# Kernel tuning notes

Measured on AMD Instinct MI355X. Metric: run time of the kernel, lower is better.

## Reference

```python
import jax, jax.numpy as jnp
import numpy as np


def setup_inputs() -> dict:
    key = jax.random.key(0)
    k1, k2, k3, k4, k5 = jax.random.split(key, 5)
    B, S, ENC, DEC = 32, 2048, 1024, 512
    hidden = jax.random.normal(k1, (B, DEC), dtype=jnp.float32)
    encoder_outputs = jax.random.normal(k2, (B, S, ENC), dtype=jnp.float32)
    W = jax.random.normal(k3, (DEC, ENC + DEC), dtype=jnp.float32) * (1.0 / np.sqrt(ENC + DEC))
    b = jax.random.normal(k4, (DEC,), dtype=jnp.float32) * 0.01
    v = jax.random.uniform(k5, (DEC,), dtype=jnp.float32)  # torch.rand init
    return {"hidden": hidden, "encoder_outputs": encoder_outputs, "W": W, "b": b, "v": v}


def reference(hidden, encoder_outputs, W, b, v):
    # hidden: [B, D_dec], encoder_outputs: [B, S, D_enc]
    # Concat order in original: (hidden, encoder_outputs) -> split W accordingly.
    D_dec = hidden.shape[-1]
    Wh = W[:, :D_dec]   # [D_dec, D_dec] acts on hidden
    We = W[:, D_dec:]   # [D_dec, D_enc] acts on encoder_outputs
    # energy: tanh(Linear(cat(hidden_repeated, enc))) == tanh(h@Wh^T + enc@We^T + b)
    h_proj = jnp.einsum('bd,ed->be', hidden, Wh)                 # [B, D_dec]
    e_proj = jnp.einsum('bse,de->bsd', encoder_outputs, We)      # [B, S, D_dec]
    energy = jnp.tanh(e_proj + h_proj[:, None, :] + b)           # [B, S, D_dec]
    # scores: v . energy per (b, s); softmax over src_len
    scores = jnp.einsum('d,bsd->bs', v, energy)                  # [B, S]
    attn = jax.nn.softmax(scores, axis=-1)
    return attn[:, None, :]                                       # [B, 1, S]
```

## Files before the change

### kernel.cpp

```cpp
#include <hip/hip_runtime.h>
#include <hip/hip_bf16.h>


typedef __attribute__((ext_vector_type(8))) short bf16x8;
typedef __attribute__((ext_vector_type(4))) float f32x4;

__device__ __forceinline__ ushort f2bf(float x) {
    __hip_bfloat16 h = __float2bfloat16(x);
    return *reinterpret_cast<ushort*>(&h);
}

__device__ __forceinline__ bf16x8 pack8(float4 a, float4 b) {
    bf16x8 o;
    o[0] = (short)f2bf(a.x); o[1] = (short)f2bf(a.y);
    o[2] = (short)f2bf(a.z); o[3] = (short)f2bf(a.w);
    o[4] = (short)f2bf(b.x); o[5] = (short)f2bf(b.y);
    o[6] = (short)f2bf(b.z); o[7] = (short)f2bf(b.w);
    return o;
}

#define WS_WBF   0
#define WS_HB    (1u << 20)
#define WS_SCORE ((1u << 20) + (64u << 10))

__global__ void prep_kernel(const float* __restrict__ W,
                            const float* __restrict__ hidden,
                            const float* __restrict__ bias,
                            ushort* __restrict__ Wbf,
                            float* __restrict__ hb,
                            float* __restrict__ score) {
    const int bid = blockIdx.x, tid = threadIdx.x;
    if (bid < 512) {
        int idx = bid * 256 + tid;
        int d  = idx >> 8;
        int e4 = (idx & 255) * 4;
        float4 f = *(const float4*)(W + (size_t)d * 1536 + 512 + e4);
        ushort4 u;
        u.x = f2bf(f.x); u.y = f2bf(f.y); u.z = f2bf(f.z); u.w = f2bf(f.w);
        *(ushort4*)(Wbf + (size_t)d * 1024 + e4) = u;
    } else if (bid < 576) {
        int idx = (bid - 512) * 256 + tid;
        int b = idx >> 9, d = idx & 511;
        const float4* hp = (const float4*)(hidden + b * 512);
        const float4* wp = (const float4*)(W + (size_t)d * 1536);
        float acc = 0.f;
#pragma unroll 8
        for (int j = 0; j < 128; ++j) {
            float4 h = hp[j], w = wp[j];
            acc += h.x * w.x + h.y * w.y + h.z * w.z + h.w * w.w;
        }
        hb[idx] = acc + bias[d];
    } else {
        int idx = (bid - 576) * 256 + tid;
        float4 z = {0.f, 0.f, 0.f, 0.f};
        *(float4*)(score + (size_t)idx * 4) = z;
    }
}

__launch_bounds__(256, 3)
__global__ void eproj_scores(const float* __restrict__ enc,
                             const ushort* __restrict__ Wbf,
                             const float* __restrict__ hb,
                             const float* __restrict__ v,
                             float* __restrict__ scores) {
    __shared__ alignas(16) float Abuf[2][128 * 32];
    __shared__ float spart[2][128];

    const int tid  = threadIdx.x;
    const int lane = tid & 63, w = tid >> 6;
    const int wm = w >> 1, wn = w & 1;
    const int q = lane >> 4, ln = lane & 15;
    const int  nblk = blockIdx.x & 3;
    const long m0   = (long)(blockIdx.x >> 2) * 128;
    const int  bidx = (int)(m0 >> 11);
    const int  n0   = nblk * 128 + wn * 64;

    f32x4 acc[4][4];
#pragma unroll
    for (int mt = 0; mt < 4; ++mt)
#pragma unroll
        for (int nt = 0; nt < 4; ++nt)
            acc[mt][nt] = (f32x4){0.f, 0.f, 0.f, 0.f};

    const ushort* bptr[4];
#pragma unroll
    for (int nt = 0; nt < 4; ++nt)
        bptr[nt] = Wbf + (size_t)(n0 + nt * 16 + ln) * 1024 + q * 8;

    int sA0[4], sA1[4];
#pragma unroll
    for (int mt = 0; mt < 4; ++mt) {
        int rA = wm * 64 + mt * 16 + ln;
        sA0[mt] = (rA * 8 + ((2 * q)     ^ (rA & 7))) * 4;
        sA1[mt] = (rA * 8 + ((2 * q + 1) ^ (rA & 7))) * 4;
    }

#pragma unroll
    for (int i = 0; i < 4; ++i) {
        int s = i * 256 + tid;
        int r = s >> 3;
        int c = (s & 7) ^ (r & 7);
        const float* g = enc + (m0 + r) * 1024 + c * 4;
        float* lb = &Abuf[0][(i * 256 + w * 64) * 4];
        __builtin_amdgcn_global_load_lds(
            (const __attribute__((address_space(1))) void*)g,
            (__attribute__((address_space(3))) void*)lb, 16, 0, 0);
    }
    bf16x8 bfr[2][4];
#pragma unroll
    for (int nt = 0; nt < 4; ++nt)
        bfr[0][nt] = *(const bf16x8*)(bptr[nt]);

    int buf = 0;
#pragma unroll 2
    for (int kt = 0; kt < 32; ++kt) {
        const int p = kt & 1;
        __syncthreads();

        if (kt < 31) {
#pragma unroll
            for (int i = 0; i < 4; ++i) {
                int s = i * 256 + tid;
                int r = s >> 3;
                int c = (s & 7) ^ (r & 7);
                const float* g = enc + (m0 + r) * 1024 + (kt + 1) * 32 + c * 4;
                float* lb = &Abuf[buf ^ 1][(i * 256 + w * 64) * 4];
                __builtin_amdgcn_global_load_lds(
                    (const __attribute__((address_space(1))) void*)g,
                    (__attribute__((address_space(3))) void*)lb, 16, 0, 0);
            }
#pragma unroll
            for (int nt = 0; nt < 4; ++nt)
                bfr[p ^ 1][nt] = *(const bf16x8*)(bptr[nt] + (size_t)(kt + 1) * 32);
        }

        const float* Ab = Abuf[buf];
#pragma unroll
        for (int mt = 0; mt < 4; ++mt) {
            float4 a0 = *(const float4*)(Ab + sA0[mt]);
            float4 a1 = *(const float4*)(Ab + sA1[mt]);
            bf16x8 af = pack8(a0, a1);
#pragma unroll
            for (int nt = 0; nt < 4; ++nt)
                acc[mt][nt] = __builtin_amdgcn_mfma_f32_16x16x32_bf16(
                    af, bfr[p][nt], acc[mt][nt], 0, 0, 0);
        }
        buf ^= 1;
    }

    float partial[4][4];
#pragma unroll
    for (int mt = 0; mt < 4; ++mt)
#pragma unroll
        for (int r = 0; r < 4; ++r) partial[mt][r] = 0.f;

#pragma unroll
    for (int nt = 0; nt < 4; ++nt) {
        int d = n0 + nt * 16 + ln;
        float hbv = hb[bidx * 512 + d];
        float vv  = v[d];
#pragma unroll
        for (int mt = 0; mt < 4; ++mt)
#pragma unroll
            for (int r = 0; r < 4; ++r) {
                float x = acc[mt][nt][r] + hbv;
                float e = __expf(2.f * x);
                partial[mt][r] += vv * (1.f - 2.f / (e + 1.f));
            }
    }
#pragma unroll
    for (int mt = 0; mt < 4; ++mt)
#pragma unroll
        for (int r = 0; r < 4; ++r) {
            float s = partial[mt][r];
            s += __shfl_xor(s, 1);
            s += __shfl_xor(s, 2);
            s += __shfl_xor(s, 4);
            s += __shfl_xor(s, 8);
            partial[mt][r] = s;
        }
    if (ln == 0) {
#pragma unroll
        for (int mt = 0; mt < 4; ++mt)
#pragma unroll
            for (int r = 0; r < 4; ++r)
                spart[wn][wm * 64 + mt * 16 + q * 4 + r] = partial[mt][r];
    }
    __syncthreads();
    if (tid < 128)
        atomicAdd(&scores[m0 + tid], spart[0][tid] + spart[1][tid]);
}

__global__ void softmax_kernel(const float* __restrict__ scores, float* __restrict__ out) {
    int b = blockIdx.x;
    const float* sc = scores + b * 2048;
    __shared__ float wred[4], wsum[4];

    float lmax = -1e30f;
    for (int i = threadIdx.x; i < 2048; i += 256) lmax = fmaxf(lmax, sc[i]);
#pragma unroll
    for (int m = 1; m < 64; m <<= 1) lmax = fmaxf(lmax, __shfl_xor(lmax, m));
    if ((threadIdx.x & 63) == 0) wred[threadIdx.x >> 6] = lmax;
    __syncthreads();
    float gmax = fmaxf(fmaxf(wred[0], wred[1]), fmaxf(wred[2], wred[3]));

    float lsum = 0.f;
    for (int i = threadIdx.x; i < 2048; i += 256) lsum += __expf(sc[i] - gmax);
#pragma unroll
    for (int m = 1; m < 64; m <<= 1) lsum += __shfl_xor(lsum, m);
    if ((threadIdx.x & 63) == 0) wsum[threadIdx.x >> 6] = lsum;
    __syncthreads();
    float inv = 1.f / (wsum[0] + wsum[1] + wsum[2] + wsum[3]);

    for (int i = threadIdx.x; i < 2048; i += 256)
        out[b * 2048 + i] = __expf(sc[i] - gmax) * inv;
}

extern "C" void kernel_launch(void* const* d_in, const int* in_sizes, int n_in,
                              void* d_out, int out_size, void* d_ws, size_t ws_size,
                              hipStream_t stream) {
    const float* hidden = (const float*)d_in[0];
    const float* enc    = (const float*)d_in[1];
    const float* W      = (const float*)d_in[2];
    const float* bias   = (const float*)d_in[3];
    const float* v      = (const float*)d_in[4];
    float* out = (float*)d_out;

    char* ws = (char*)d_ws;
    ushort* Wbf   = (ushort*)(ws + WS_WBF);
    float*  hb    = (float*)(ws + WS_HB);
    float*  score = (float*)(ws + WS_SCORE);

    hipLaunchKernelGGL(prep_kernel,  dim3(640),  dim3(256), 0, stream,
                       W, hidden, bias, Wbf, hb, score);
    hipLaunchKernelGGL(eproj_scores, dim3(2048), dim3(256), 0, stream,
                       enc, Wbf, hb, v, score);
    hipLaunchKernelGGL(softmax_kernel, dim3(32), dim3(256), 0, stream, score, out);
}
```

Baseline: 508.5 us.

## Retile eproj GEMM to 64x256 blocks with 4-stage grouped LDS prefetch

Changes each block to cover 64 rows by 256 output columns, so all four waves share one encoder tile and each encoder row is read by two blocks instead of four. Loads are grouped into 128-wide k-chunks, double-buffered across two 32 KB halves, which cuts barriers from 32 to 8. Trades higher LDS use (64 KB, occupancy limited to two blocks) for less global traffic on the dominant fp32 input; the score partial buffer reuses the A buffer after a barrier.

```diff
diff --git a/kernel.cpp b/kernel.cpp
--- a/kernel.cpp
+++ b/kernel.cpp
@@ -57,23 +57,21 @@
     }
 }
 
-__launch_bounds__(256, 3)
+__launch_bounds__(256, 2)
 __global__ void eproj_scores(const float* __restrict__ enc,
                              const ushort* __restrict__ Wbf,
                              const float* __restrict__ hb,
                              const float* __restrict__ v,
                              float* __restrict__ scores) {
-    __shared__ alignas(16) float Abuf[2][128 * 32];
-    __shared__ float spart[2][128];
+    __shared__ alignas(16) float Abuf[2][4][2048];
 
     const int tid  = threadIdx.x;
     const int lane = tid & 63, w = tid >> 6;
-    const int wm = w >> 1, wn = w & 1;
     const int q = lane >> 4, ln = lane & 15;
-    const int  nblk = blockIdx.x & 3;
-    const long m0   = (long)(blockIdx.x >> 2) * 128;
+    const int  nblk = blockIdx.x & 1;
+    const long m0   = (long)(blockIdx.x >> 1) * 64;
     const int  bidx = (int)(m0 >> 11);
-    const int  n0   = nblk * 128 + wn * 64;
+    const int  n0   = nblk * 256 + w * 64;
 
     f32x4 acc[4][4];
 #pragma unroll
@@ -90,62 +88,59 @@
     int sA0[4], sA1[4];
 #pragma unroll
     for (int mt = 0; mt < 4; ++mt) {
-        int rA = wm * 64 + mt * 16 + ln;
+        int rA = mt * 16 + ln;
         sA0[mt] = (rA * 8 + ((2 * q)     ^ (rA & 7))) * 4;
         sA1[mt] = (rA * 8 + ((2 * q + 1) ^ (rA & 7))) * 4;
     }
 
-#pragma unroll
-    for (int i = 0; i < 4; ++i) {
-        int s = i * 256 + tid;
-        int r = s >> 3;
-        int c = (s & 7) ^ (r & 7);
-        const float* g = enc + (m0 + r) * 1024 + c * 4;
-        float* lb = &Abuf[0][(i * 256 + w * 64) * 4];
-        __builtin_amdgcn_global_load_lds(
-            (const __attribute__((address_space(1))) void*)g,
-            (__attribute__((address_space(3))) void*)lb, 16, 0, 0);
-    }
-    bf16x8 bfr[2][4];
-#pragma unroll
-    for (int nt = 0; nt < 4; ++nt)
-        bfr[0][nt] = *(const bf16x8*)(bptr[nt]);
-
-    int buf = 0;
-#pragma unroll 2
-    for (int kt = 0; kt < 32; ++kt) {
-        const int p = kt & 1;
-        __syncthreads();
-
-        if (kt < 31) {
-#pragma unroll
-            for (int i = 0; i < 4; ++i) {
+    auto dma_group = [&](int h, int k0) {
+#pragma unroll
+        for (int st = 0; st < 4; ++st)
+#pragma unroll
+            for (int i = 0; i < 2; ++i) {
                 int s = i * 256 + tid;
                 int r = s >> 3;
                 int c = (s & 7) ^ (r & 7);
-                const float* g = enc + (m0 + r) * 1024 + (kt + 1) * 32 + c * 4;
-                float* lb = &Abuf[buf ^ 1][(i * 256 + w * 64) * 4];
+                const float* g = enc + (m0 + r) * 1024 + k0 + st * 32 + c * 4;
+                float* lb = &Abuf[h][st][(i * 256 + w * 64) * 4];
                 __builtin_amdgcn_global_load_lds(
                     (const __attribute__((address_space(1))) void*)g,
                     (__attribute__((address_space(3))) void*)lb, 16, 0, 0);
             }
-#pragma unroll
-            for (int nt = 0; nt < 4; ++nt)
-                bfr[p ^ 1][nt] = *(const bf16x8*)(bptr[nt] + (size_t)(kt + 1) * 32);
+    };
+
+    dma_group(0, 0);
+    bf16x8 bfr[2][4];
+#pragma unroll
+    for (int nt = 0; nt < 4; ++nt)
+        bfr[0][nt] = *(const bf16x8*)(bptr[nt]);
+
+    for (int g = 0; g < 8; ++g) {
+        __syncthreads();
+        if (g < 7) dma_group((g + 1) & 1, (g + 1) * 128);
+
+        const float* H = &Abuf[g & 1][0][0];
+#pragma unroll
+        for (int j = 0; j < 4; ++j) {
+            const int kt = g * 4 + j;
+            if (kt < 31) {
+#pragma unroll
+                for (int nt = 0; nt < 4; ++nt)
+                    bfr[(j + 1) & 1][nt] =
+                        *(const bf16x8*)(bptr[nt] + (size_t)(kt + 1) * 32);
+            }
+            const float* Ab = H + j * 2048;
+#pragma unroll
+            for (int mt = 0; mt < 4; ++mt) {
+                float4 a0 = *(const float4*)(Ab + sA0[mt]);
+                float4 a1 = *(const float4*)(Ab + sA1[mt]);
+                bf16x8 af = pack8(a0, a1);
+#pragma unroll
+                for (int nt = 0; nt < 4; ++nt)
+                    acc[mt][nt] = __builtin_amdgcn_mfma_f32_16x16x32_bf16(
+                        af, bfr[j & 1][nt], acc[mt][nt], 0, 0, 0);
+            }
         }
-
-        const float* Ab = Abuf[buf];
-#pragma unroll
-        for (int mt = 0; mt < 4; ++mt) {
-            float4 a0 = *(const float4*)(Ab + sA0[mt]);
-            float4 a1 = *(const float4*)(Ab + sA1[mt]);
-            bf16x8 af = pack8(a0, a1);
-#pragma unroll
-            for (int nt = 0; nt < 4; ++nt)
-                acc[mt][nt] = __builtin_amdgcn_mfma_f32_16x16x32_bf16(
-                    af, bfr[p][nt], acc[mt][nt], 0, 0, 0);
-        }
-        buf ^= 1;
     }
 
     float partial[4][4];
@@ -179,16 +174,20 @@
             s += __shfl_xor(s, 8);
             partial[mt][r] = s;
         }
+
+    __syncthreads();
+    float* spart = (float*)Abuf;
     if (ln == 0) {
 #pragma unroll
         for (int mt = 0; mt < 4; ++mt)
 #pragma unroll
             for (int r = 0; r < 4; ++r)
-                spart[wn][wm * 64 + mt * 16 + q * 4 + r] = partial[mt][r];
-    }
-    __syncthreads();
-    if (tid < 128)
-        atomicAdd(&scores[m0 + tid], spart[0][tid] + spart[1][tid]);
+                spart[w * 64 + mt * 16 + q * 4 + r] = partial[mt][r];
+    }
+    __syncthreads();
+    if (tid < 64)
+        atomicAdd(&scores[m0 + tid],
+                  spart[tid] + spart[64 + tid] + spart[128 + tid] + spart[192 + tid]);
 }
 
 __global__ void softmax_kernel(const float* __restrict__ scores, float* __restrict__ out) {
```

After: 488.5 us. -3.9%, faster.
